# Optimization experiments

Measured on AMD Instinct MI355X. Metric: run time of the kernel, lower is better.

Reference implementation:

```python
import jax, jax.numpy as jnp
import numpy as np
import math

N_HEAD = 16
N_KV_HEAD = 4
N_EMBD = 2048
HEAD_DIM = N_EMBD // N_HEAD  # 128
SCALE = 1.0 / math.sqrt(HEAD_DIM)
B, T = 2, 2048


def setup_inputs() -> dict:
    key = jax.random.key(0)
    ks = jax.random.split(key, 5)
    s = 0.02
    x = jax.random.normal(ks[0], (B, T, N_EMBD), dtype=jnp.float32)
    wq = jax.random.normal(ks[1], (N_EMBD, N_EMBD), dtype=jnp.float32) * s
    wk = jax.random.normal(ks[2], (N_KV_HEAD * HEAD_DIM, N_EMBD), dtype=jnp.float32) * s
    wv = jax.random.normal(ks[3], (N_KV_HEAD * HEAD_DIM, N_EMBD), dtype=jnp.float32) * s
    wo = jax.random.normal(ks[4], (N_EMBD, N_EMBD), dtype=jnp.float32) * s
    return {"x": x, "wq": wq, "wk": wk, "wv": wv, "wo": wo}


def _forward(x, wq, wk, wv, wo):
    b, t, _ = x.shape
    # Linear layers: y = x @ W.T  (torch Linear weight is (out,in))
    q = (x @ wq.T).reshape(b, t, N_HEAD, HEAD_DIM).transpose(0, 2, 1, 3)      # (B,H,T,D)
    k = (x @ wk.T).reshape(b, t, N_KV_HEAD, HEAD_DIM).transpose(0, 2, 1, 3)  # (B,Hkv,T,D)
    v = (x @ wv.T).reshape(b, t, N_KV_HEAD, HEAD_DIM).transpose(0, 2, 1, 3)
    groups = N_HEAD // N_KV_HEAD
    k = jnp.repeat(k, groups, axis=1)  # repeat_interleave over head dim -> (B,H,T,D)
    v = jnp.repeat(v, groups, axis=1)
    # Causal mask: True above diagonal (masked-out positions)
    mask = jnp.triu(jnp.ones((t, t), dtype=bool), k=1)[None, None]  # (1,1,T,T)
    scores = jnp.einsum('bhqd,bhkd->bhqk', q, k) * SCALE
    scores = jnp.where(mask, -jnp.inf, scores)
    attn = jax.nn.softmax(scores, axis=-1)
    attn = jnp.where(mask, 0.0, attn)
    y = jnp.einsum('bhqk,bhkd->bhqd', attn, v)       # (B,H,T,D)
    y = y.transpose(0, 2, 1, 3).reshape(b, t, N_EMBD)
    return y @ wo.T


def reference(x, wq, wk, wv, wo):
    return _forward(x, wq, wk, wv, wo)
```

## Files before the change

### kernel.cpp

```cpp
#include <hip/hip_runtime.h>
#include <cstdint>
#include <cstddef>

typedef __bf16 bf16_t;
typedef __bf16 bf16x8 __attribute__((ext_vector_type(8)));
typedef __bf16 bf16x4 __attribute__((ext_vector_type(4)));
typedef float f32x4 __attribute__((ext_vector_type(4)));

#define GL2LDS16(gptr, lptr)                                                   \
  __builtin_amdgcn_global_load_lds(                                            \
      (__attribute__((address_space(1))) void*)(gptr),                         \
      (__attribute__((address_space(3))) void*)(lptr), 16, 0, 0)

__device__ __forceinline__ float fast_exp2(float x) {
  float r;
  asm volatile("v_exp_f32 %0, %1" : "=v"(r) : "v"(x));
  return r;
}

#define BATCH 2
#define T_SEQ 2048
#define NH 16
#define NKV 4
#define HD 128
#define EMB 2048
#define KVDIM (NKV * HD)
#define MROWS (BATCH * T_SEQ)

__global__ void cvt_all(const float4* __restrict__ x,  const float4* __restrict__ wq,
                        const float4* __restrict__ wk, const float4* __restrict__ wv,
                        const float4* __restrict__ wo,
                        bf16x4* __restrict__ xb,  bf16x4* __restrict__ wqb,
                        bf16x4* __restrict__ wkb, bf16x4* __restrict__ wvb,
                        bf16x4* __restrict__ wob) {
  const int blk = blockIdx.x;
  const float4* src;
  bf16x4* dst;
  int base;
  if (blk < 8192)       { src = x;  dst = xb;  base = blk; }
  else if (blk < 12288) { src = wq; dst = wqb; base = blk - 8192; }
  else if (blk < 13312) { src = wk; dst = wkb; base = blk - 12288; }
  else if (blk < 14336) { src = wv; dst = wvb; base = blk - 13312; }
  else                  { src = wo; dst = wob; base = blk - 14336; }
  const int i = base * 256 + threadIdx.x;
  const float4 v = src[i];
  dst[i] = bf16x4{(__bf16)v.x, (__bf16)v.y, (__bf16)v.z, (__bf16)v.w};
}

#define BK8 64
#define NT8 (EMB / BK8)

__global__ __launch_bounds__(512, 2)
void gemm_qkv8(const bf16_t* __restrict__ A,
               const bf16_t* __restrict__ Wq, const bf16_t* __restrict__ Wk,
               const bf16_t* __restrict__ Wv,
               bf16_t* __restrict__ Qb, bf16_t* __restrict__ Kb,
               bf16_t* __restrict__ Vt, float qalpha)
{
  __shared__ bf16_t lds[2][512 * 64];

  const int tid  = threadIdx.x;
  const int lane = tid & 63;
  const int wv   = tid >> 6;
  const int l15  = lane & 15;
  const int lq   = lane >> 4;

  const int bid0 = blockIdx.x;
  const int bid  = (bid0 & 7) * 24 + (bid0 >> 3);
  const int mt = bid / 12, nt = bid % 12;
  const int m0 = mt * 256;

  const bf16_t* Bmat; int ncol0, seg;
  if (nt < 8)       { Bmat = Wq; ncol0 = nt * 256;        seg = 0; }
  else if (nt < 10) { Bmat = Wk; ncol0 = (nt - 8) * 256;  seg = 1; }
  else              { Bmat = Wv; ncol0 = (nt - 10) * 256; seg = 2; }

  const int wm = (wv >> 2) * 128;
  const int wn = (wv & 3) * 64;

  f32x4 acc[8][4] = {};

  auto stage = [&](int dbuf, int tsrc, int h) {
    const int k0 = tsrc * BK8;
    const bf16_t* src = (h < 2) ? A : Bmat;
    const int rbase = (h < 2) ? (m0 + h * 128) : (ncol0 + (h - 2) * 128);
    bf16_t* dst = &lds[dbuf][h * 8192];
#pragma unroll
    for (int r = 0; r < 2; ++r) {
      const int c = r * 512 + tid;
      const int row = c >> 3, p = c & 7;
      const int sb = p ^ (row & 7);
      GL2LDS16(src + (size_t)(rbase + row) * EMB + k0 + sb * 8, dst + c * 8);
    }
  };

  stage(0, 0, 0); stage(0, 0, 1); stage(0, 0, 2); stage(0, 0, 3);
  stage(1, 1, 2); stage(1, 1, 0); stage(1, 1, 3);
  asm volatile("s_waitcnt vmcnt(6)" ::: "memory");
  __builtin_amdgcn_s_barrier();

  bf16x8 a[4][2], b[4][2];

#pragma unroll 1
  for (int tt = 0; tt < NT8; tt += 2) {
#pragma unroll
    for (int u = 0; u < 2; ++u) {
      const int t   = tt + u;
      const int cur = u;
      const int nxt = u ^ 1;
      const int tn1 = (t + 1 < NT8) ? t + 1 : NT8 - 1;
      const int tn2 = (t + 2 < NT8) ? t + 2 : NT8 - 1;

#pragma unroll
      for (int i = 0; i < 4; ++i) {
        const int row = wm + i * 16 + l15;
#pragma unroll
        for (int ks = 0; ks < 2; ++ks)
          a[i][ks] = *(const bf16x8*)&lds[cur][row * 64 + (((ks * 4 + lq) ^ (row & 7)) * 8)];
      }
#pragma unroll
      for (int j = 0; j < 2; ++j) {
        const int row = 256 + wn + j * 16 + l15;
#pragma unroll
        for (int ks = 0; ks < 2; ++ks)
          b[j][ks] = *(const bf16x8*)&lds[cur][row * 64 + (((ks * 4 + lq) ^ (row & 7)) * 8)];
      }
      stage(nxt, tn1, 1);
      __builtin_amdgcn_s_barrier();
      __builtin_amdgcn_s_setprio(1);
#pragma unroll
      for (int ks = 0; ks < 2; ++ks)
#pragma unroll
        for (int i = 0; i < 4; ++i)
#pragma unroll
          for (int j = 0; j < 2; ++j)
            acc[i][j] = __builtin_amdgcn_mfma_f32_16x16x32_bf16(a[i][ks], b[j][ks], acc[i][j], 0, 0, 0);
      __builtin_amdgcn_s_setprio(0);
      __builtin_amdgcn_s_barrier();

#pragma unroll
      for (int j = 2; j < 4; ++j) {
        const int row = 256 + wn + j * 16 + l15;
#pragma unroll
        for (int ks = 0; ks < 2; ++ks)
          b[j][ks] = *(const bf16x8*)&lds[cur][row * 64 + (((ks * 4 + lq) ^ (row & 7)) * 8)];
      }
      __builtin_amdgcn_s_barrier();
      __builtin_amdgcn_s_setprio(1);
#pragma unroll
      for (int ks = 0; ks < 2; ++ks)
#pragma unroll
        for (int i = 0; i < 4; ++i)
#pragma unroll
          for (int j = 2; j < 4; ++j)
            acc[i][j] = __builtin_amdgcn_mfma_f32_16x16x32_bf16(a[i][ks], b[j][ks], acc[i][j], 0, 0, 0);
      __builtin_amdgcn_s_setprio(0);
      __builtin_amdgcn_s_barrier();

#pragma unroll
      for (int i = 0; i < 4; ++i) {
        const int row = wm + (4 + i) * 16 + l15;
#pragma unroll
        for (int ks = 0; ks < 2; ++ks)
          a[i][ks] = *(const bf16x8*)&lds[cur][row * 64 + (((ks * 4 + lq) ^ (row & 7)) * 8)];
      }
      stage(cur, tn2, 2);
      __builtin_amdgcn_s_barrier();
      __builtin_amdgcn_s_setprio(1);
#pragma unroll
      for (int ks = 0; ks < 2; ++ks)
#pragma unroll
        for (int i = 0; i < 4; ++i)
#pragma unroll
          for (int j = 2; j < 4; ++j)
            acc[4 + i][j] = __builtin_amdgcn_mfma_f32_16x16x32_bf16(a[i][ks], b[j][ks], acc[4 + i][j], 0, 0, 0);
      __builtin_amdgcn_s_setprio(0);
      __builtin_amdgcn_s_barrier();

      stage(cur, tn2, 0);
      stage(cur, tn2, 3);
      __builtin_amdgcn_s_barrier();
      __builtin_amdgcn_s_setprio(1);
#pragma unroll
      for (int ks = 0; ks < 2; ++ks)
#pragma unroll
        for (int i = 0; i < 4; ++i)
#pragma unroll
          for (int j = 0; j < 2; ++j)
            acc[4 + i][j] = __builtin_amdgcn_mfma_f32_16x16x32_bf16(a[i][ks], b[j][ks], acc[4 + i][j], 0, 0, 0);
      __builtin_amdgcn_s_setprio(0);
      asm volatile("s_waitcnt vmcnt(6)" ::: "memory");
      __builtin_amdgcn_s_barrier();
    }
  }
  asm volatile("s_waitcnt vmcnt(0)" ::: "memory");

  if (seg == 0) {
#pragma unroll
    for (int i = 0; i < 8; ++i) {
      const int rbase = m0 + wm + i * 16 + lq * 4;
#pragma unroll
      for (int j = 0; j < 4; ++j) {
        const int col = ncol0 + wn + j * 16 + l15;
#pragma unroll
        for (int r = 0; r < 4; ++r)
          Qb[(size_t)(rbase + r) * EMB + col] = (bf16_t)(acc[i][j][r] * qalpha);
      }
    }
  } else if (seg == 1) {
#pragma unroll
    for (int i = 0; i < 8; ++i) {
      const int rbase = m0 + wm + i * 16 + lq * 4;
#pragma unroll
      for (int j = 0; j < 4; ++j) {
        const int col = ncol0 + wn + j * 16 + l15;
#pragma unroll
        for (int r = 0; r < 4; ++r)
          Kb[(size_t)(rbase + r) * KVDIM + col] = (bf16_t)acc[i][j][r];
      }
    }
  } else {
    const int bb = m0 >> 11;
    const int mloc0 = (m0 & 2047) + wm + lq * 4;
#pragma unroll
    for (int i = 0; i < 8; ++i) {
      const int mloc = mloc0 + i * 16;
#pragma unroll
      for (int j = 0; j < 4; ++j) {
        const int d = ncol0 + wn + j * 16 + l15;
        *(bf16x4*)(Vt + (size_t)(bb * KVDIM + d) * T_SEQ + mloc) =
            bf16x4{(__bf16)acc[i][j][0], (__bf16)acc[i][j][1],
                   (__bf16)acc[i][j][2], (__bf16)acc[i][j][3]};
      }
    }
  }
}

__global__ __launch_bounds__(256, 2)
void gemm_out(const bf16_t* __restrict__ A, const bf16_t* __restrict__ Bm,
              float* __restrict__ C, int M, int N, int K)
{
  __shared__ bf16_t As[128 * 64];
  __shared__ bf16_t Bs[128 * 64];

  const int tid  = threadIdx.x;
  const int lane = tid & 63;
  const int wv   = tid >> 6;
  const int m0 = blockIdx.y * 128;
  const int n0 = blockIdx.x * 128;
  const int wm = (wv >> 1) * 64;
  const int wn = (wv & 1) * 64;
  const int l15 = lane & 15;
  const int lq  = lane >> 4;

  f32x4 acc[4][4] = {};
  const int srow = tid >> 3;
  const int scol = (tid & 7) * 8;

  for (int k0 = 0; k0 < K; k0 += 64) {
#pragma unroll
    for (int r = 0; r < 4; ++r) {
      const int row = r * 32 + srow;
      GL2LDS16(A + (size_t)(m0 + row) * K + k0 + scol, As + row * 64 + scol);
    }
#pragma unroll
    for (int r = 0; r < 4; ++r) {
      const int row = r * 32 + srow;
      GL2LDS16(Bm + (size_t)(n0 + row) * K + k0 + scol, Bs + row * 64 + scol);
    }
    __syncthreads();

#pragma unroll
    for (int ks = 0; ks < 2; ++ks) {
      const int kc = ks * 32 + lq * 8;
      bf16x8 af[4], bf[4];
#pragma unroll
      for (int i = 0; i < 4; ++i)
        af[i] = *(const bf16x8*)(As + (wm + i * 16 + l15) * 64 + kc);
#pragma unroll
      for (int j = 0; j < 4; ++j)
        bf[j] = *(const bf16x8*)(Bs + (wn + j * 16 + l15) * 64 + kc);
#pragma unroll
      for (int i = 0; i < 4; ++i)
#pragma unroll
        for (int j = 0; j < 4; ++j)
          acc[i][j] = __builtin_amdgcn_mfma_f32_16x16x32_bf16(af[i], bf[j], acc[i][j], 0, 0, 0);
    }
    __syncthreads();
  }

#pragma unroll
  for (int i = 0; i < 4; ++i) {
    const int rbase = m0 + wm + i * 16 + lq * 4;
#pragma unroll
    for (int j = 0; j < 4; ++j) {
      const int col = n0 + wn + j * 16 + l15;
#pragma unroll
      for (int r = 0; r < 4; ++r)
        C[(size_t)(rbase + r) * N + col] = acc[i][j][r];
    }
  }
}

#define PSTR 72

__global__ __launch_bounds__(256, 1)
void attn_fwd(const bf16_t* __restrict__ Q, const bf16_t* __restrict__ Kg,
              const bf16_t* __restrict__ Vt, bf16_t* __restrict__ Y)
{
  __shared__ bf16_t Ks[2][64 * 128];
  __shared__ bf16_t Vs[2][128 * 64];
  __shared__ bf16_t Ps[4][32 * PSTR];

  const int tid  = threadIdx.x;
  const int lane = tid & 63;
  const int wv   = tid >> 6;
  const int l15  = lane & 15;
  const int lq   = lane >> 4;
  const int h  = blockIdx.y;
  const int b  = blockIdx.z;
  const int hkv = h >> 2;
  bf16_t* Psw = Ps[wv];

  auto stage = [&](int kt, int bufsel) {
    const int base_t = b * T_SEQ + kt * 64;
#pragma unroll
    for (int r = 0; r < 4; ++r) {
      const int c = r * 256 + tid;
      const int row = c >> 4, p = c & 15;
      const int sb = p ^ (row & 7);
      GL2LDS16(Kg + (size_t)(base_t + row) * KVDIM + hkv * HD + sb * 8,
               &Ks[bufsel][c * 8]);
    }
#pragma unroll
    for (int r = 0; r < 4; ++r) {
      const int c = r * 256 + tid;
      const int row = c >> 3, p = c & 7;
      const int sb = p ^ (row & 7);
      GL2LDS16(Vt + (size_t)(b * KVDIM + hkv * HD + row) * T_SEQ + kt * 64 + sb * 8,
               &Vs[bufsel][c * 8]);
    }
  };

#pragma unroll 1
  for (int ph = 0; ph < 2; ++ph) {
    const int qt = ph ? blockIdx.x : (15 - blockIdx.x);
    const int q0 = qt * 128;
    const int nkt = 2 * qt + 2;
    const int qa0 = q0 + wv * 32 + l15;
    const int qa1 = qa0 + 16;

    bf16x8 qf0[4], qf1[4];
    {
      const bf16_t* qp0 = Q + ((size_t)(b * T_SEQ + qa0) * NH + h) * HD + lq * 8;
      const bf16_t* qp1 = Q + ((size_t)(b * T_SEQ + qa1) * NH + h) * HD + lq * 8;
#pragma unroll
      for (int ds = 0; ds < 4; ++ds) {
        qf0[ds] = *(const bf16x8*)(qp0 + ds * 32);
        qf1[ds] = *(const bf16x8*)(qp1 + ds * 32);
      }
    }

    float l0 = 0.f, l1 = 0.f;
    f32x4 o0[8], o1[8];
#pragma unroll
    for (int nb = 0; nb < 8; ++nb) {
      o0[nb] = f32x4{0.f, 0.f, 0.f, 0.f};
      o1[nb] = f32x4{0.f, 0.f, 0.f, 0.f};
    }

    __syncthreads();
    stage(0, 0);

    for (int kt = 0; kt < nkt; ++kt) {
      const int cur = kt & 1;
      __syncthreads();
      if (kt + 1 < nkt) stage(kt + 1, cur ^ 1);

      f32x4 s0[4], s1[4];
#pragma unroll
      for (int nb = 0; nb < 4; ++nb) {
        s0[nb] = f32x4{0.f, 0.f, 0.f, 0.f};
        s1[nb] = f32x4{0.f, 0.f, 0.f, 0.f};
        const int row = nb * 16 + l15;
        const int r7  = row & 7;
#pragma unroll
        for (int ds = 0; ds < 4; ++ds) {
          const bf16x8 kf = *(const bf16x8*)&Ks[cur][row * 128 + (((ds * 4 + lq) ^ r7) * 8)];
          s0[nb] = __builtin_amdgcn_mfma_f32_16x16x32_bf16(kf, qf0[ds], s0[nb], 0, 0, 0);
          s1[nb] = __builtin_amdgcn_mfma_f32_16x16x32_bf16(kf, qf1[ds], s1[nb], 0, 0, 0);
        }
      }

      const bool dia = (kt >= nkt - 2);
#pragma unroll
      for (int nb = 0; nb < 4; ++nb) {
        const int kvb = kt * 64 + nb * 16 + lq * 4;
        float p0, p1, p2, p3;
        if (dia) {
          p0 = (kvb + 0 <= qa0) ? fast_exp2(s0[nb][0]) : 0.f;
          p1 = (kvb + 1 <= qa0) ? fast_exp2(s0[nb][1]) : 0.f;
          p2 = (kvb + 2 <= qa0) ? fast_exp2(s0[nb][2]) : 0.f;
          p3 = (kvb + 3 <= qa0) ? fast_exp2(s0[nb][3]) : 0.f;
        } else {
          p0 = fast_exp2(s0[nb][0]);
          p1 = fast_exp2(s0[nb][1]);
          p2 = fast_exp2(s0[nb][2]);
          p3 = fast_exp2(s0[nb][3]);
        }
        l0 += (p0 + p1) + (p2 + p3);
        *(bf16x4*)(Psw + l15 * PSTR + nb * 16 + lq * 4) =
            bf16x4{(__bf16)p0, (__bf16)p1, (__bf16)p2, (__bf16)p3};

        if (dia) {
          p0 = (kvb + 0 <= qa1) ? fast_exp2(s1[nb][0]) : 0.f;
          p1 = (kvb + 1 <= qa1) ? fast_exp2(s1[nb][1]) : 0.f;
          p2 = (kvb + 2 <= qa1) ? fast_exp2(s1[nb][2]) : 0.f;
          p3 = (kvb + 3 <= qa1) ? fast_exp2(s1[nb][3]) : 0.f;
        } else {
          p0 = fast_exp2(s1[nb][0]);
          p1 = fast_exp2(s1[nb][1]);
          p2 = fast_exp2(s1[nb][2]);
          p3 = fast_exp2(s1[nb][3]);
        }
        l1 += (p0 + p1) + (p2 + p3);
        *(bf16x4*)(Psw + (16 + l15) * PSTR + nb * 16 + lq * 4) =
            bf16x4{(__bf16)p0, (__bf16)p1, (__bf16)p2, (__bf16)p3};
      }

      asm volatile("s_waitcnt lgkmcnt(0)" ::: "memory");

#pragma unroll
      for (int ks = 0; ks < 2; ++ks) {
        const bf16x8 pf0 = *(const bf16x8*)(Psw + l15 * PSTR + ks * 32 + lq * 8);
        const bf16x8 pf1 = *(const bf16x8*)(Psw + (16 + l15) * PSTR + ks * 32 + lq * 8);
#pragma unroll
        for (int nb = 0; nb < 8; ++nb) {
          const int row = nb * 16 + l15;
          const bf16x8 vf = *(const bf16x8*)&Vs[cur][row * 64 + (((ks * 4 + lq) ^ (row & 7)) * 8)];
          o0[nb] = __builtin_amdgcn_mfma_f32_16x16x32_bf16(vf, pf0, o0[nb], 0, 0, 0);
          o1[nb] = __builtin_amdgcn_mfma_f32_16x16x32_bf16(vf, pf1, o1[nb], 0, 0, 0);
        }
      }
    }

    float lt0 = l0, lt1 = l1;
    lt0 += __shfl_xor(lt0, 16);
    lt0 += __shfl_xor(lt0, 32);
    lt1 += __shfl_xor(lt1, 16);
    lt1 += __shfl_xor(lt1, 32);
    const float inv0 = 1.f / lt0;
    const float inv1 = 1.f / lt1;
    bf16_t* yp0 = Y + ((size_t)(b * T_SEQ + qa0) * NH + h) * HD + lq * 4;
    bf16_t* yp1 = Y + ((size_t)(b * T_SEQ + qa1) * NH + h) * HD + lq * 4;
#pragma unroll
    for (int nb = 0; nb < 8; ++nb) {
      *(bf16x4*)(yp0 + nb * 16) = bf16x4{(__bf16)(o0[nb][0] * inv0), (__bf16)(o0[nb][1] * inv0),
                                         (__bf16)(o0[nb][2] * inv0), (__bf16)(o0[nb][3] * inv0)};
      *(bf16x4*)(yp1 + nb * 16) = bf16x4{(__bf16)(o1[nb][0] * inv1), (__bf16)(o1[nb][1] * inv1),
                                         (__bf16)(o1[nb][2] * inv1), (__bf16)(o1[nb][3] * inv1)};
    }
  }
}

extern "C" void kernel_launch(void* const* d_in, const int* in_sizes, int n_in,
                              void* d_out, int out_size, void* d_ws, size_t ws_size,
                              hipStream_t stream) {
  const float* x  = (const float*)d_in[0];
  const float* wq = (const float*)d_in[1];
  const float* wk = (const float*)d_in[2];
  const float* wv = (const float*)d_in[3];
  const float* wo = (const float*)d_in[4];
  float* out = (float*)d_out;

  const size_t n_x  = (size_t)MROWS * EMB;
  const size_t n_wq = (size_t)EMB * EMB;
  const size_t n_wk = (size_t)KVDIM * EMB;

  bf16_t* xb  = (bf16_t*)d_ws;
  bf16_t* wqb = xb  + n_x;
  bf16_t* wkb = wqb + n_wq;
  bf16_t* wvb = wkb + n_wk;
  bf16_t* wob = wvb + n_wk;
  bf16_t* Qb  = wob + n_wq;
  bf16_t* Kb  = Qb + (size_t)MROWS * EMB;
  bf16_t* Vtb = Kb + (size_t)MROWS * KVDIM;
  bf16_t* Yb  = Vtb + (size_t)MROWS * KVDIM;

  dim3 blk(256);

  cvt_all<<<dim3(18432), blk, 0, stream>>>(
      (const float4*)x, (const float4*)wq, (const float4*)wk, (const float4*)wv, (const float4*)wo,
      (bf16x4*)xb, (bf16x4*)wqb, (bf16x4*)wkb, (bf16x4*)wvb, (bf16x4*)wob);

  const float qalpha = 0.08838834764831845f * 1.4426950408889634f;
  gemm_qkv8<<<dim3(192), dim3(512), 0, stream>>>(xb, wqb, wkb, wvb,
                                                 Qb, Kb, Vtb, qalpha);

  attn_fwd<<<dim3(8, NH, BATCH), blk, 0, stream>>>(Qb, Kb, Vtb, Yb);

  gemm_out<<<dim3(EMB / 128, MROWS / 128), blk, 0, stream>>>(Yb, wob, out, MROWS, EMB, EMB);
}
```

Measured before the change: 301.9 us.

## Split attention kv tile into halves, one q-tile per block, two blocks per CU

The attention kernel stops pairing two causal q-tiles per block and instead launches one block per q-tile (16 along x), with launch bounds raised to two blocks per CU. Each 64-key tile is processed as two 32-key halves, and the second half's QK MFMAs are issued before the first half's PV MFMAs so the exp/softmax work can overlap matrix ops. The P scratch buffer shrinks to 32 columns, which lowers LDS use. In exchange, load balance across causal tiles now depends on the hardware scheduler, and the tighter register budget for two blocks per CU may cause spills.

```diff
diff --git a/kernel.cpp b/kernel.cpp
--- a/kernel.cpp
+++ b/kernel.cpp
@@ -302,9 +302,9 @@
   }
 }
 
-#define PSTR 72
-
-__global__ __launch_bounds__(256, 1)
+#define PSTR 40
+
+__global__ __launch_bounds__(256, 2)
 void attn_fwd(const bf16_t* __restrict__ Q, const bf16_t* __restrict__ Kg,
               const bf16_t* __restrict__ Vt, bf16_t* __restrict__ Y)
 {
@@ -342,124 +342,172 @@
     }
   };
 
-#pragma unroll 1
-  for (int ph = 0; ph < 2; ++ph) {
-    const int qt = ph ? blockIdx.x : (15 - blockIdx.x);
-    const int q0 = qt * 128;
-    const int nkt = 2 * qt + 2;
-    const int qa0 = q0 + wv * 32 + l15;
-    const int qa1 = qa0 + 16;
-
-    bf16x8 qf0[4], qf1[4];
+  const int qt  = 15 - blockIdx.x;
+  const int q0  = qt * 128;
+  const int nkt = 2 * qt + 2;
+  const int qa0 = q0 + wv * 32 + l15;
+  const int qa1 = qa0 + 16;
+
+  bf16x8 qf0[4], qf1[4];
+  {
+    const bf16_t* qp0 = Q + ((size_t)(b * T_SEQ + qa0) * NH + h) * HD + lq * 8;
+    const bf16_t* qp1 = Q + ((size_t)(b * T_SEQ + qa1) * NH + h) * HD + lq * 8;
+#pragma unroll
+    for (int ds = 0; ds < 4; ++ds) {
+      qf0[ds] = *(const bf16x8*)(qp0 + ds * 32);
+      qf1[ds] = *(const bf16x8*)(qp1 + ds * 32);
+    }
+  }
+
+  float l0 = 0.f, l1 = 0.f;
+  f32x4 o0[8], o1[8];
+#pragma unroll
+  for (int nb = 0; nb < 8; ++nb) {
+    o0[nb] = f32x4{0.f, 0.f, 0.f, 0.f};
+    o1[nb] = f32x4{0.f, 0.f, 0.f, 0.f};
+  }
+
+  stage(0, 0);
+
+  for (int kt = 0; kt < nkt; ++kt) {
+    const int cur = kt & 1;
+    __syncthreads();
+    if (kt + 1 < nkt) stage(kt + 1, cur ^ 1);
+    const bool dia = (kt >= nkt - 2);
+
+    f32x4 sA0[2], sA1[2];
+#pragma unroll
+    for (int nb = 0; nb < 2; ++nb) {
+      sA0[nb] = f32x4{0.f, 0.f, 0.f, 0.f};
+      sA1[nb] = f32x4{0.f, 0.f, 0.f, 0.f};
+      const int row = nb * 16 + l15;
+      const int r7  = row & 7;
+#pragma unroll
+      for (int ds = 0; ds < 4; ++ds) {
+        const bf16x8 kf = *(const bf16x8*)&Ks[cur][row * 128 + (((ds * 4 + lq) ^ r7) * 8)];
+        sA0[nb] = __builtin_amdgcn_mfma_f32_16x16x32_bf16(kf, qf0[ds], sA0[nb], 0, 0, 0);
+        sA1[nb] = __builtin_amdgcn_mfma_f32_16x16x32_bf16(kf, qf1[ds], sA1[nb], 0, 0, 0);
+      }
+    }
+#pragma unroll
+    for (int nb = 0; nb < 2; ++nb) {
+      const int kvb = kt * 64 + nb * 16 + lq * 4;
+      float p0, p1, p2, p3;
+      if (dia) {
+        p0 = (kvb + 0 <= qa0) ? fast_exp2(sA0[nb][0]) : 0.f;
+        p1 = (kvb + 1 <= qa0) ? fast_exp2(sA0[nb][1]) : 0.f;
+        p2 = (kvb + 2 <= qa0) ? fast_exp2(sA0[nb][2]) : 0.f;
+        p3 = (kvb + 3 <= qa0) ? fast_exp2(sA0[nb][3]) : 0.f;
+      } else {
+        p0 = fast_exp2(sA0[nb][0]); p1 = fast_exp2(sA0[nb][1]);
+        p2 = fast_exp2(sA0[nb][2]); p3 = fast_exp2(sA0[nb][3]);
+      }
+      l0 += (p0 + p1) + (p2 + p3);
+      *(bf16x4*)(Psw + l15 * PSTR + nb * 16 + lq * 4) =
+          bf16x4{(__bf16)p0, (__bf16)p1, (__bf16)p2, (__bf16)p3};
+
+      if (dia) {
+        p0 = (kvb + 0 <= qa1) ? fast_exp2(sA1[nb][0]) : 0.f;
+        p1 = (kvb + 1 <= qa1) ? fast_exp2(sA1[nb][1]) : 0.f;
+        p2 = (kvb + 2 <= qa1) ? fast_exp2(sA1[nb][2]) : 0.f;
+        p3 = (kvb + 3 <= qa1) ? fast_exp2(sA1[nb][3]) : 0.f;
+      } else {
+        p0 = fast_exp2(sA1[nb][0]); p1 = fast_exp2(sA1[nb][1]);
+        p2 = fast_exp2(sA1[nb][2]); p3 = fast_exp2(sA1[nb][3]);
+      }
+      l1 += (p0 + p1) + (p2 + p3);
+      *(bf16x4*)(Psw + (16 + l15) * PSTR + nb * 16 + lq * 4) =
+          bf16x4{(__bf16)p0, (__bf16)p1, (__bf16)p2, (__bf16)p3};
+    }
+
+    f32x4 sB0[2], sB1[2];
+#pragma unroll
+    for (int nb = 0; nb < 2; ++nb) {
+      sB0[nb] = f32x4{0.f, 0.f, 0.f, 0.f};
+      sB1[nb] = f32x4{0.f, 0.f, 0.f, 0.f};
+      const int row = (nb + 2) * 16 + l15;
+      const int r7  = row & 7;
+#pragma unroll
+      for (int ds = 0; ds < 4; ++ds) {
+        const bf16x8 kf = *(const bf16x8*)&Ks[cur][row * 128 + (((ds * 4 + lq) ^ r7) * 8)];
+        sB0[nb] = __builtin_amdgcn_mfma_f32_16x16x32_bf16(kf, qf0[ds], sB0[nb], 0, 0, 0);
+        sB1[nb] = __builtin_amdgcn_mfma_f32_16x16x32_bf16(kf, qf1[ds], sB1[nb], 0, 0, 0);
+      }
+    }
+
+    asm volatile("s_waitcnt lgkmcnt(0)" ::: "memory");
     {
-      const bf16_t* qp0 = Q + ((size_t)(b * T_SEQ + qa0) * NH + h) * HD + lq * 8;
-      const bf16_t* qp1 = Q + ((size_t)(b * T_SEQ + qa1) * NH + h) * HD + lq * 8;
-#pragma unroll
-      for (int ds = 0; ds < 4; ++ds) {
-        qf0[ds] = *(const bf16x8*)(qp0 + ds * 32);
-        qf1[ds] = *(const bf16x8*)(qp1 + ds * 32);
-      }
-    }
-
-    float l0 = 0.f, l1 = 0.f;
-    f32x4 o0[8], o1[8];
-#pragma unroll
-    for (int nb = 0; nb < 8; ++nb) {
-      o0[nb] = f32x4{0.f, 0.f, 0.f, 0.f};
-      o1[nb] = f32x4{0.f, 0.f, 0.f, 0.f};
-    }
-
-    __syncthreads();
-    stage(0, 0);
-
-    for (int kt = 0; kt < nkt; ++kt) {
-      const int cur = kt & 1;
-      __syncthreads();
-      if (kt + 1 < nkt) stage(kt + 1, cur ^ 1);
-
-      f32x4 s0[4], s1[4];
-#pragma unroll
-      for (int nb = 0; nb < 4; ++nb) {
-        s0[nb] = f32x4{0.f, 0.f, 0.f, 0.f};
-        s1[nb] = f32x4{0.f, 0.f, 0.f, 0.f};
+      const bf16x8 pf0 = *(const bf16x8*)(Psw + l15 * PSTR + lq * 8);
+      const bf16x8 pf1 = *(const bf16x8*)(Psw + (16 + l15) * PSTR + lq * 8);
+#pragma unroll
+      for (int nb = 0; nb < 8; ++nb) {
         const int row = nb * 16 + l15;
-        const int r7  = row & 7;
-#pragma unroll
-        for (int ds = 0; ds < 4; ++ds) {
-          const bf16x8 kf = *(const bf16x8*)&Ks[cur][row * 128 + (((ds * 4 + lq) ^ r7) * 8)];
-          s0[nb] = __builtin_amdgcn_mfma_f32_16x16x32_bf16(kf, qf0[ds], s0[nb], 0, 0, 0);
-          s1[nb] = __builtin_amdgcn_mfma_f32_16x16x32_bf16(kf, qf1[ds], s1[nb], 0, 0, 0);
-        }
-      }
-
-      const bool dia = (kt >= nkt - 2);
-#pragma unroll
-      for (int nb = 0; nb < 4; ++nb) {
-        const int kvb = kt * 64 + nb * 16 + lq * 4;
-        float p0, p1, p2, p3;
-        if (dia) {
-          p0 = (kvb + 0 <= qa0) ? fast_exp2(s0[nb][0]) : 0.f;
-          p1 = (kvb + 1 <= qa0) ? fast_exp2(s0[nb][1]) : 0.f;
-          p2 = (kvb + 2 <= qa0) ? fast_exp2(s0[nb][2]) : 0.f;
-          p3 = (kvb + 3 <= qa0) ? fast_exp2(s0[nb][3]) : 0.f;
-        } else {
-          p0 = fast_exp2(s0[nb][0]);
-          p1 = fast_exp2(s0[nb][1]);
-          p2 = fast_exp2(s0[nb][2]);
-          p3 = fast_exp2(s0[nb][3]);
-        }
-        l0 += (p0 + p1) + (p2 + p3);
-        *(bf16x4*)(Psw + l15 * PSTR + nb * 16 + lq * 4) =
-            bf16x4{(__bf16)p0, (__bf16)p1, (__bf16)p2, (__bf16)p3};
-
-        if (dia) {
-          p0 = (kvb + 0 <= qa1) ? fast_exp2(s1[nb][0]) : 0.f;
-          p1 = (kvb + 1 <= qa1) ? fast_exp2(s1[nb][1]) : 0.f;
-          p2 = (kvb + 2 <= qa1) ? fast_exp2(s1[nb][2]) : 0.f;
-          p3 = (kvb + 3 <= qa1) ? fast_exp2(s1[nb][3]) : 0.f;
-        } else {
-          p0 = fast_exp2(s1[nb][0]);
-          p1 = fast_exp2(s1[nb][1]);
-          p2 = fast_exp2(s1[nb][2]);
-          p3 = fast_exp2(s1[nb][3]);
-        }
-        l1 += (p0 + p1) + (p2 + p3);
-        *(bf16x4*)(Psw + (16 + l15) * PSTR + nb * 16 + lq * 4) =
-            bf16x4{(__bf16)p0, (__bf16)p1, (__bf16)p2, (__bf16)p3};
-      }
-
-      asm volatile("s_waitcnt lgkmcnt(0)" ::: "memory");
-
-#pragma unroll
-      for (int ks = 0; ks < 2; ++ks) {
-        const bf16x8 pf0 = *(const bf16x8*)(Psw + l15 * PSTR + ks * 32 + lq * 8);
-        const bf16x8 pf1 = *(const bf16x8*)(Psw + (16 + l15) * PSTR + ks * 32 + lq * 8);
-#pragma unroll
-        for (int nb = 0; nb < 8; ++nb) {
-          const int row = nb * 16 + l15;
-          const bf16x8 vf = *(const bf16x8*)&Vs[cur][row * 64 + (((ks * 4 + lq) ^ (row & 7)) * 8)];
-          o0[nb] = __builtin_amdgcn_mfma_f32_16x16x32_bf16(vf, pf0, o0[nb], 0, 0, 0);
-          o1[nb] = __builtin_amdgcn_mfma_f32_16x16x32_bf16(vf, pf1, o1[nb], 0, 0, 0);
-        }
-      }
-    }
-
-    float lt0 = l0, lt1 = l1;
-    lt0 += __shfl_xor(lt0, 16);
-    lt0 += __shfl_xor(lt0, 32);
-    lt1 += __shfl_xor(lt1, 16);
-    lt1 += __shfl_xor(lt1, 32);
-    const float inv0 = 1.f / lt0;
-    const float inv1 = 1.f / lt1;
-    bf16_t* yp0 = Y + ((size_t)(b * T_SEQ + qa0) * NH + h) * HD + lq * 4;
-    bf16_t* yp1 = Y + ((size_t)(b * T_SEQ + qa1) * NH + h) * HD + lq * 4;
-#pragma unroll
-    for (int nb = 0; nb < 8; ++nb) {
-      *(bf16x4*)(yp0 + nb * 16) = bf16x4{(__bf16)(o0[nb][0] * inv0), (__bf16)(o0[nb][1] * inv0),
-                                         (__bf16)(o0[nb][2] * inv0), (__bf16)(o0[nb][3] * inv0)};
-      *(bf16x4*)(yp1 + nb * 16) = bf16x4{(__bf16)(o1[nb][0] * inv1), (__bf16)(o1[nb][1] * inv1),
-                                         (__bf16)(o1[nb][2] * inv1), (__bf16)(o1[nb][3] * inv1)};
-    }
+        const bf16x8 vf = *(const bf16x8*)&Vs[cur][row * 64 + ((lq ^ (row & 7)) * 8)];
+        o0[nb] = __builtin_amdgcn_mfma_f32_16x16x32_bf16(vf, pf0, o0[nb], 0, 0, 0);
+        o1[nb] = __builtin_amdgcn_mfma_f32_16x16x32_bf16(vf, pf1, o1[nb], 0, 0, 0);
+      }
+    }
+
+#pragma unroll
+    for (int nb = 0; nb < 2; ++nb) {
+      const int kvb = kt * 64 + (nb + 2) * 16 + lq * 4;
+      float p0, p1, p2, p3;
+      if (dia) {
+        p0 = (kvb + 0 <= qa0) ? fast_exp2(sB0[nb][0]) : 0.f;
+        p1 = (kvb + 1 <= qa0) ? fast_exp2(sB0[nb][1]) : 0.f;
+        p2 = (kvb + 2 <= qa0) ? fast_exp2(sB0[nb][2]) : 0.f;
+        p3 = (kvb + 3 <= qa0) ? fast_exp2(sB0[nb][3]) : 0.f;
+      } else {
+        p0 = fast_exp2(sB0[nb][0]); p1 = fast_exp2(sB0[nb][1]);
+        p2 = fast_exp2(sB0[nb][2]); p3 = fast_exp2(sB0[nb][3]);
+      }
+      l0 += (p0 + p1) + (p2 + p3);
+      *(bf16x4*)(Psw + l15 * PSTR + nb * 16 + lq * 4) =
+          bf16x4{(__bf16)p0, (__bf16)p1, (__bf16)p2, (__bf16)p3};
+
+      if (dia) {
+        p0 = (kvb + 0 <= qa1) ? fast_exp2(sB1[nb][0]) : 0.f;
+        p1 = (kvb + 1 <= qa1) ? fast_exp2(sB1[nb][1]) : 0.f;
+        p2 = (kvb + 2 <= qa1) ? fast_exp2(sB1[nb][2]) : 0.f;
+        p3 = (kvb + 3 <= qa1) ? fast_exp2(sB1[nb][3]) : 0.f;
+      } else {
+        p0 = fast_exp2(sB1[nb][0]); p1 = fast_exp2(sB1[nb][1]);
+        p2 = fast_exp2(sB1[nb][2]); p3 = fast_exp2(sB1[nb][3]);
+      }
+      l1 += (p0 + p1) + (p2 + p3);
+      *(bf16x4*)(Psw + (16 + l15) * PSTR + nb * 16 + lq * 4) =
+          bf16x4{(__bf16)p0, (__bf16)p1, (__bf16)p2, (__bf16)p3};
+    }
+
+    asm volatile("s_waitcnt lgkmcnt(0)" ::: "memory");
+    {
+      const bf16x8 pf0 = *(const bf16x8*)(Psw + l15 * PSTR + lq * 8);
+      const bf16x8 pf1 = *(const bf16x8*)(Psw + (16 + l15) * PSTR + lq * 8);
+#pragma unroll
+      for (int nb = 0; nb < 8; ++nb) {
+        const int row = nb * 16 + l15;
+        const bf16x8 vf = *(const bf16x8*)&Vs[cur][row * 64 + ((((4 + lq)) ^ (row & 7)) * 8)];
+        o0[nb] = __builtin_amdgcn_mfma_f32_16x16x32_bf16(vf, pf0, o0[nb], 0, 0, 0);
+        o1[nb] = __builtin_amdgcn_mfma_f32_16x16x32_bf16(vf, pf1, o1[nb], 0, 0, 0);
+      }
+    }
+  }
+
+  float lt0 = l0, lt1 = l1;
+  lt0 += __shfl_xor(lt0, 16);
+  lt0 += __shfl_xor(lt0, 32);
+  lt1 += __shfl_xor(lt1, 16);
+  lt1 += __shfl_xor(lt1, 32);
+  const float inv0 = 1.f / lt0;
+  const float inv1 = 1.f / lt1;
+  bf16_t* yp0 = Y + ((size_t)(b * T_SEQ + qa0) * NH + h) * HD + lq * 4;
+  bf16_t* yp1 = Y + ((size_t)(b * T_SEQ + qa1) * NH + h) * HD + lq * 4;
+#pragma unroll
+  for (int nb = 0; nb < 8; ++nb) {
+    *(bf16x4*)(yp0 + nb * 16) = bf16x4{(__bf16)(o0[nb][0] * inv0), (__bf16)(o0[nb][1] * inv0),
+                                       (__bf16)(o0[nb][2] * inv0), (__bf16)(o0[nb][3] * inv0)};
+    *(bf16x4*)(yp1 + nb * 16) = bf16x4{(__bf16)(o1[nb][0] * inv1), (__bf16)(o1[nb][1] * inv1),
+                                       (__bf16)(o1[nb][2] * inv1), (__bf16)(o1[nb][3] * inv1)};
   }
 }
 
@@ -497,7 +545,7 @@
   gemm_qkv8<<<dim3(192), dim3(512), 0, stream>>>(xb, wqb, wkb, wvb,
                                                  Qb, Kb, Vtb, qalpha);
 
-  attn_fwd<<<dim3(8, NH, BATCH), blk, 0, stream>>>(Qb, Kb, Vtb, Yb);
+  attn_fwd<<<dim3(16, NH, BATCH), blk, 0, stream>>>(Qb, Kb, Vtb, Yb);
 
   gemm_out<<<dim3(EMB / 128, MROWS / 128), blk, 0, stream>>>(Yb, wob, out, MROWS, EMB, EMB);
 }
```

Result: no change. 301.8 us (-0.0%).
